# Optimization experiments

Hardware: AMD Instinct MI355X
Metric: run time of the kernel (lower is better)

Reference implementation:

```python
import jax, jax.numpy as jnp
import numpy as np

NEG_CLAMP = -100.0  # torch BCE clamps log terms at -100


def cxcywh_to_xyxy(b):
    cx, cy, w, h = b[..., 0], b[..., 1], b[..., 2], b[..., 3]
    return jnp.stack([cx - 0.5 * w, cy - 0.5 * h, cx + 0.5 * w, cy + 0.5 * h], axis=-1)


def generalized_box_iou(a, b):
    # a: [N,4], b: [T,4] in xyxy
    area_a = (a[:, 2] - a[:, 0]) * (a[:, 3] - a[:, 1])
    area_b = (b[:, 2] - b[:, 0]) * (b[:, 3] - b[:, 1])
    lt = jnp.maximum(a[:, None, :2], b[None, :, :2])
    rb = jnp.minimum(a[:, None, 2:], b[None, :, 2:])
    wh = jnp.clip(rb - lt, 0.0)
    inter = wh[..., 0] * wh[..., 1]
    union = area_a[:, None] + area_b[None, :] - inter
    iou = inter / union
    ltc = jnp.minimum(a[:, None, :2], b[None, :, :2])
    rbc = jnp.maximum(a[:, None, 2:], b[None, :, 2:])
    whc = jnp.clip(rbc - ltc, 0.0)
    areac = whc[..., 0] * whc[..., 1]
    return iou - (areac - union) / areac


def setup_inputs() -> dict:
    key = jax.random.key(0)
    k0, k1, k2, k3, k4, k5 = jax.random.split(key, 6)
    bs, Q, C = 4, 300, 80
    T = 200  # 50 targets per image
    H = W = 160
    H2 = W2 = 320
    pred_logits = jax.random.normal(k0, (bs, Q, C), dtype=jnp.float32)
    pred_boxes = jax.random.uniform(k1, (bs, Q, 4), dtype=jnp.float32, minval=0.02, maxval=0.98)
    pred_masks = jax.random.normal(k2, (bs, Q, H, W), dtype=jnp.float32)
    tgt_ids = jax.random.randint(k3, (T,), 0, C)
    tgt_bbox = jax.random.uniform(k4, (T, 4), dtype=jnp.float32, minval=0.02, maxval=0.98)
    tgt_masks = jnp.round(jax.random.uniform(k5, (T, H2, W2), dtype=jnp.float32))  # binary masks
    return {"pred_logits": pred_logits, "pred_boxes": pred_boxes, "pred_masks": pred_masks,
            "tgt_ids": tgt_ids, "tgt_bbox": tgt_bbox, "tgt_masks": tgt_masks}


def reference(pred_logits, pred_boxes, pred_masks, tgt_ids, tgt_bbox, tgt_masks):
    cost_class_w, cost_bbox_w, cost_giou_w, cost_mask_w, cost_dice_w = 2.0, 5.0, 2.0, 2.0, 2.0
    bs, Q = pred_logits.shape[:2]
    N = bs * Q
    T = tgt_bbox.shape[0]

    out_prob = jax.nn.sigmoid(pred_logits.reshape(N, -1))      # [N, C]
    out_bbox = pred_boxes.reshape(N, 4)

    cost_class = -out_prob[:, tgt_ids]                           # [N, T] gather
    cost_bbox = jnp.abs(out_bbox[:, None, :] - tgt_bbox[None, :, :]).sum(-1)  # L1 cdist
    cost_giou = -generalized_box_iou(cxcywh_to_xyxy(out_bbox), cxcywh_to_xyxy(tgt_bbox))

    C = cost_bbox_w * cost_bbox + cost_giou_w * cost_giou + cost_class_w * cost_class

    # mask costs
    H, W = pred_masks.shape[-2:]
    HW = H * W
    out_logits = pred_masks.reshape(N, HW)
    out_flat = jax.nn.sigmoid(out_logits)                        # [N, HW]
    tgt_resized = jax.image.resize(tgt_masks, (T, H, W), method='bilinear')  # align_corners=False
    tgt_flat = tgt_resized.reshape(T, HW)

    numerator = 2.0 * (out_flat @ tgt_flat.T)                    # [N, T]
    denominator = out_flat.sum(-1)[:, None] + tgt_flat.sum(-1)[None, :]
    cost_dice = -(numerator + 1.0) / (jnp.clip(denominator, 1e-6) + 1.0)

    # BCE mean over pixels as pairwise matmuls (same math as the expanded torch version)
    log_p = jnp.maximum(jax.nn.log_sigmoid(out_logits), NEG_CLAMP)       # log(p)
    log_1mp = jnp.maximum(jax.nn.log_sigmoid(-out_logits), NEG_CLAMP)    # log(1-p)
    cost_mask = -(log_p @ tgt_flat.T + log_1mp @ (1.0 - tgt_flat).T) / HW

    C = C + cost_mask_w * cost_mask + cost_dice_w * cost_dice
    return C.reshape(bs, Q, T)
```

## Files before the change

kernel.cpp:

```cpp
#include <hip/hip_runtime.h>
#include <math.h>

#define N_PRED 1200
#define N_TGT  200
#define T_PAD  208
#define NCLS   80
#define W_OUT  160
#define W_IN   320
#define HW     25600
#define K_TOT  25600
#define KS     25
#define K_CHUNK 1024
#define BK     64
#define MT     19
#define LDA    72
#define LDB    72

typedef __bf16 bf16x8 __attribute__((ext_vector_type(8)));
typedef float  f32x4  __attribute__((ext_vector_type(4)));

__device__ __forceinline__ unsigned short f2bf(float f) {
    unsigned int u = __float_as_uint(f);
    u = u + 0x7FFFu + ((u >> 16) & 1u);
    return (unsigned short)(u >> 16);
}

__device__ __forceinline__ void taps(int i, int& i0, float w[4]) {
    if (i == 0)            { i0 = 0;       w[0]=3.f/7.f; w[1]=3.f/7.f; w[2]=1.f/7.f; w[3]=0.f; }
    else if (i == W_OUT-1) { i0 = 2*i - 2; w[0]=0.f;     w[1]=1.f/7.f; w[2]=3.f/7.f; w[3]=3.f/7.f; }
    else                   { i0 = 2*i - 1; w[0]=0.125f;  w[1]=0.375f;  w[2]=0.375f;  w[3]=0.125f; }
}

__global__ void resize_kernel(const float* __restrict__ tm,
                              unsigned short* __restrict__ tgt_bf,
                              float* __restrict__ tgt_sum) {
    const int t = blockIdx.y, q = blockIdx.x, tid = threadIdx.x;
    if (t >= N_TGT) {
        uint4 z = make_uint4(0,0,0,0);
        uint4* dst = (uint4*)(tgt_bf + (size_t)t * HW) + q * (HW/8/4);
        for (int u = tid; u < HW/8/4; u += 256) dst[u] = z;
        return;
    }
    const float* src = tm + (size_t)t * (W_IN * W_IN);
    float part = 0.f;
    const int p0 = q * (HW/4);
    for (int pp = tid; pp < HW/4; pp += 256) {
        const int p = p0 + pp;
        const int i = p / W_OUT, j = p % W_OUT;
        int r0, c0; float wr[4], wc[4];
        taps(i, r0, wr); taps(j, c0, wc);
        float v = 0.f;
        #pragma unroll
        for (int a = 0; a < 4; a++) {
            const float* row = src + (size_t)(r0 + a) * W_IN + c0;
            float h = wc[0]*row[0] + wc[1]*row[1] + wc[2]*row[2] + wc[3]*row[3];
            v += wr[a] * h;
        }
        tgt_bf[(size_t)t * HW + p] = f2bf(v);
        part += v;
    }
    __shared__ float red[256];
    red[tid] = part; __syncthreads();
    for (int s = 128; s > 0; s >>= 1) { if (tid < s) red[tid] += red[tid + s]; __syncthreads(); }
    if (tid == 0) atomicAdd(&tgt_sum[t], red[0]);
}

__global__ void rowsum_kernel(const float* __restrict__ pm,
                              float* __restrict__ sig_rs,
                              float* __restrict__ l1p_rs) {
    const int n = blockIdx.x, tid = threadIdx.x;
    const float* row = pm + (size_t)n * HW;
    float s = 0.f, l = 0.f;
    #pragma unroll
    for (int i = 0; i < 25; i++) {
        float4 x4 = *(const float4*)(row + tid * 4 + i * 1024);
        float xs[4] = {x4.x, x4.y, x4.z, x4.w};
        #pragma unroll
        for (int e = 0; e < 4; e++) {
            const float xv = xs[e];
            const float t  = __expf(-fabsf(xv));
            const float inv = __builtin_amdgcn_rcpf(1.f + t);
            s += (xv >= 0.f) ? inv : (1.f - inv);
            l -= __logf(1.f + t) + fmaxf(xv, 0.f);
        }
    }
    __shared__ float redS[256], redL[256];
    redS[tid] = s; redL[tid] = l; __syncthreads();
    for (int st = 128; st > 0; st >>= 1) {
        if (tid < st) { redS[tid] += redS[tid + st]; redL[tid] += redL[tid + st]; }
        __syncthreads();
    }
    if (tid == 0) { sig_rs[n] = redS[0]; l1p_rs[n] = redL[0]; }
}

#define DECL13(p) f32x4 p##0={0,0,0,0}, p##1={0,0,0,0}, p##2={0,0,0,0}, p##3={0,0,0,0}, \
    p##4={0,0,0,0}, p##5={0,0,0,0}, p##6={0,0,0,0}, p##7={0,0,0,0}, p##8={0,0,0,0}, \
    p##9={0,0,0,0}, p##10={0,0,0,0}, p##11={0,0,0,0}, p##12={0,0,0,0}

#define STEP(tt) { bf16x8 b = *(const bf16x8*)&ldsB[((tt)*16 + l16) * LDB + koff]; \
    accS##tt = __builtin_amdgcn_mfma_f32_16x16x32_bf16(aS, b, accS##tt, 0, 0, 0); \
    accX##tt = __builtin_amdgcn_mfma_f32_16x16x32_bf16(aX, b, accX##tt, 0, 0, 0); }

#define CONVW(J, RA) { \
    const float x0 = RA.x, x1 = RA.y, x2 = RA.z, x3 = RA.w; \
    const float s0 = __builtin_amdgcn_rcpf(1.f + __expf(-x0)); \
    const float s1 = __builtin_amdgcn_rcpf(1.f + __expf(-x1)); \
    const float s2 = __builtin_amdgcn_rcpf(1.f + __expf(-x2)); \
    const float s3 = __builtin_amdgcn_rcpf(1.f + __expf(-x3)); \
    const unsigned px0 = (unsigned)f2bf(x0) | ((unsigned)f2bf(x1) << 16); \
    const unsigned px1 = (unsigned)f2bf(x2) | ((unsigned)f2bf(x3) << 16); \
    const unsigned ps0 = (unsigned)f2bf(s0) | ((unsigned)f2bf(s1) << 16); \
    const unsigned ps1 = (unsigned)f2bf(s2) | ((unsigned)f2bf(s3) << 16); \
    *(uint2*)&ldsAX[((J)*16 + arow) * LDA + ac * 4] = make_uint2(px0, px1); \
    *(uint2*)&ldsAS[((J)*16 + arow) * LDA + ac * 4] = make_uint2(ps0, ps1); }

#define EPI(tt) { const size_t b0 = base + (size_t)(wave * 16 + quad * 4) * T_PAD + (tt) * 16 + l16; \
    P1[b0] = accS##tt[0]; P1[b0 + T_PAD] = accS##tt[1]; \
    P1[b0 + 2*T_PAD] = accS##tt[2]; P1[b0 + 3*T_PAD] = accS##tt[3]; \
    P2[b0] = accX##tt[0]; P2[b0 + T_PAD] = accX##tt[1]; \
    P2[b0 + 2*T_PAD] = accX##tt[2]; P2[b0 + 3*T_PAD] = accX##tt[3]; }

__global__ __launch_bounds__(256, 2)
void gemm_kernel(const float* __restrict__ pm,
                 const unsigned short* __restrict__ tgt_bf,
                 float* __restrict__ P1, float* __restrict__ P2) {
    const int ks = blockIdx.x, mtile = blockIdx.y;
    const int tid = threadIdx.x;
    const int wave = tid >> 6, lane = tid & 63;
    const int quad = lane >> 4, l16 = lane & 15;

    __shared__ unsigned short ldsAX[64 * LDA];
    __shared__ unsigned short ldsAS[64 * LDA];
    __shared__ unsigned short ldsB[T_PAD * LDB];

    DECL13(accS);
    DECL13(accX);

    const int m0 = mtile * 64;
    const int arow = tid >> 4;
    const int ac   = tid & 15;
    const int k0   = ks * K_CHUNK;

    int r0i = m0 + 0*16 + arow; if (r0i > N_PRED-1) r0i = N_PRED-1;
    int r1i = m0 + 1*16 + arow; if (r1i > N_PRED-1) r1i = N_PRED-1;
    int r2i = m0 + 2*16 + arow; if (r2i > N_PRED-1) r2i = N_PRED-1;
    int r3i = m0 + 3*16 + arow; if (r3i > N_PRED-1) r3i = N_PRED-1;
    const float* ap0 = pm + (size_t)r0i * K_TOT + ac * 4;
    const float* ap1 = pm + (size_t)r1i * K_TOT + ac * 4;
    const float* ap2 = pm + (size_t)r2i * K_TOT + ac * 4;
    const float* ap3 = pm + (size_t)r3i * K_TOT + ac * 4;

    const int bu  = tid;

    float4 rA0 = *(const float4*)(ap0 + k0);
    float4 rA1 = *(const float4*)(ap1 + k0);
    float4 rA2 = *(const float4*)(ap2 + k0);
    float4 rA3 = *(const float4*)(ap3 + k0);
    uint4 rB0, rB1, rB2, rB3, rB4, rB5, rB6;
    {
        const unsigned short* bp = tgt_bf + k0;
        rB0 = *(const uint4*)(bp + (size_t)((bu       ) >> 3) * K_TOT + ((bu       ) & 7) * 8);
        rB1 = *(const uint4*)(bp + (size_t)((bu +  256) >> 3) * K_TOT + ((bu +  256) & 7) * 8);
        rB2 = *(const uint4*)(bp + (size_t)((bu +  512) >> 3) * K_TOT + ((bu +  512) & 7) * 8);
        rB3 = *(const uint4*)(bp + (size_t)((bu +  768) >> 3) * K_TOT + ((bu +  768) & 7) * 8);
        rB4 = *(const uint4*)(bp + (size_t)((bu + 1024) >> 3) * K_TOT + ((bu + 1024) & 7) * 8);
        rB5 = *(const uint4*)(bp + (size_t)((bu + 1280) >> 3) * K_TOT + ((bu + 1280) & 7) * 8);
        if (tid < 128)
            rB6 = *(const uint4*)(bp + (size_t)((bu + 1536) >> 3) * K_TOT + ((bu + 1536) & 7) * 8);
    }

    for (int ki = 0; ki < K_CHUNK / BK; ki++) {
        __syncthreads();
        CONVW(0, rA0); CONVW(1, rA1); CONVW(2, rA2); CONVW(3, rA3);
        *(uint4*)&ldsB[((bu       ) >> 3) * LDB + ((bu       ) & 7) * 8] = rB0;
        *(uint4*)&ldsB[((bu +  256) >> 3) * LDB + ((bu +  256) & 7) * 8] = rB1;
        *(uint4*)&ldsB[((bu +  512) >> 3) * LDB + ((bu +  512) & 7) * 8] = rB2;
        *(uint4*)&ldsB[((bu +  768) >> 3) * LDB + ((bu +  768) & 7) * 8] = rB3;
        *(uint4*)&ldsB[((bu + 1024) >> 3) * LDB + ((bu + 1024) & 7) * 8] = rB4;
        *(uint4*)&ldsB[((bu + 1280) >> 3) * LDB + ((bu + 1280) & 7) * 8] = rB5;
        if (tid < 128)
            *(uint4*)&ldsB[((bu + 1536) >> 3) * LDB + ((bu + 1536) & 7) * 8] = rB6;
        __syncthreads();
        if (ki != K_CHUNK / BK - 1) {
            const int kn = k0 + (ki + 1) * BK;
            rA0 = *(const float4*)(ap0 + kn);
            rA1 = *(const float4*)(ap1 + kn);
            rA2 = *(const float4*)(ap2 + kn);
            rA3 = *(const float4*)(ap3 + kn);
            const unsigned short* bp = tgt_bf + kn;
            rB0 = *(const uint4*)(bp + (size_t)((bu       ) >> 3) * K_TOT + ((bu       ) & 7) * 8);
            rB1 = *(const uint4*)(bp + (size_t)((bu +  256) >> 3) * K_TOT + ((bu +  256) & 7) * 8);
            rB2 = *(const uint4*)(bp + (size_t)((bu +  512) >> 3) * K_TOT + ((bu +  512) & 7) * 8);
            rB3 = *(const uint4*)(bp + (size_t)((bu +  768) >> 3) * K_TOT + ((bu +  768) & 7) * 8);
            rB4 = *(const uint4*)(bp + (size_t)((bu + 1024) >> 3) * K_TOT + ((bu + 1024) & 7) * 8);
            rB5 = *(const uint4*)(bp + (size_t)((bu + 1280) >> 3) * K_TOT + ((bu + 1280) & 7) * 8);
            if (tid < 128)
                rB6 = *(const uint4*)(bp + (size_t)((bu + 1536) >> 3) * K_TOT + ((bu + 1536) & 7) * 8);
        }
        #pragma unroll
        for (int kk = 0; kk < 2; kk++) {
            const int koff = kk * 32 + quad * 8;
            bf16x8 aX = *(const bf16x8*)&ldsAX[(wave * 16 + l16) * LDA + koff];
            bf16x8 aS = *(const bf16x8*)&ldsAS[(wave * 16 + l16) * LDA + koff];
            STEP(0); STEP(1); STEP(2); STEP(3); STEP(4); STEP(5); STEP(6);
            STEP(7); STEP(8); STEP(9); STEP(10); STEP(11); STEP(12);
        }
    }
    const size_t base = ((size_t)(mtile * KS + ks)) * 64 * T_PAD;
    EPI(0); EPI(1); EPI(2); EPI(3); EPI(4); EPI(5); EPI(6);
    EPI(7); EPI(8); EPI(9); EPI(10); EPI(11); EPI(12);
}

__global__ void combine_kernel(const float* __restrict__ pred_logits,
                               const float* __restrict__ pred_boxes,
                               const int*   __restrict__ tgt_ids,
                               const float* __restrict__ tgt_bbox,
                               const float* __restrict__ P1, const float* __restrict__ P2,
                               const float* __restrict__ sig_rs, const float* __restrict__ l1p_rs,
                               const float* __restrict__ tgt_sum,
                               float* __restrict__ out) {
    const int e = blockIdx.x * 256 + threadIdx.x;
    if (e >= N_PRED * N_TGT) return;
    const int n = e / N_TGT, t = e - n * N_TGT;
    const int mtile = n >> 6, mrow = n & 63;

    const size_t pb = ((size_t)mtile * KS * 64 + mrow) * T_PAD + t;
    float s1 = 0.f, s2 = 0.f;
    for (int ks = 0; ks < KS; ks++) {
        s1 += P1[pb + (size_t)ks * 64 * T_PAD];
        s2 += P2[pb + (size_t)ks * 64 * T_PAD];
    }
    const float denom = sig_rs[n] + tgt_sum[t];
    const float cost_dice = -(2.f * s1 + 1.f) / (fmaxf(denom, 1e-6f) + 1.f);
    const float cost_mask = -(s2 + l1p_rs[n]) / (float)HW;
    const int id = tgt_ids[t];
    const float lg = pred_logits[(size_t)n * NCLS + id];
    const float p = 1.f / (1.f + __expf(-lg));
    const float4 ob = *(const float4*)(pred_boxes + (size_t)n * 4);
    const float4 tb = *(const float4*)(tgt_bbox + (size_t)t * 4);
    const float l1 = fabsf(ob.x - tb.x) + fabsf(ob.y - tb.y) + fabsf(ob.z - tb.z) + fabsf(ob.w - tb.w);
    const float ax0 = ob.x - 0.5f*ob.z, ay0 = ob.y - 0.5f*ob.w;
    const float ax1 = ob.x + 0.5f*ob.z, ay1 = ob.y + 0.5f*ob.w;
    const float bx0 = tb.x - 0.5f*tb.z, by0 = tb.y - 0.5f*tb.w;
    const float bx1 = tb.x + 0.5f*tb.z, by1 = tb.y + 0.5f*tb.w;
    const float areaA = (ax1 - ax0) * (ay1 - ay0);
    const float areaB = (bx1 - bx0) * (by1 - by0);
    const float iw = fmaxf(fminf(ax1, bx1) - fmaxf(ax0, bx0), 0.f);
    const float ih = fmaxf(fminf(ay1, by1) - fmaxf(ay0, by0), 0.f);
    const float inter = iw * ih;
    const float uni = areaA + areaB - inter;
    const float iou = inter / uni;
    const float cw = fmaxf(fmaxf(ax1, bx1) - fminf(ax0, bx0), 0.f);
    const float ch = fmaxf(fmaxf(ay1, by1) - fminf(ay0, by0), 0.f);
    const float areaC = cw * ch;
    const float giou = iou - (areaC - uni) / areaC;

    out[e] = 5.f * l1 + 2.f * (-giou) + 2.f * (-p) + 2.f * cost_mask + 2.f * cost_dice;
}

extern "C" void kernel_launch(void* const* d_in, const int* in_sizes, int n_in,
                              void* d_out, int out_size, void* d_ws, size_t ws_size,
                              hipStream_t stream) {
    const float* pred_logits = (const float*)d_in[0];
    const float* pred_boxes  = (const float*)d_in[1];
    const float* pred_masks  = (const float*)d_in[2];
    const int*   tgt_ids     = (const int*)d_in[3];
    const float* tgt_bbox    = (const float*)d_in[4];
    const float* tgt_masks   = (const float*)d_in[5];
    float* out = (float*)d_out;

    char* ws = (char*)d_ws;
    size_t off = 0;
    unsigned short* tgt_bf = (unsigned short*)(ws + off);
    off += (size_t)T_PAD * K_TOT * sizeof(unsigned short);
    off = (off + 255) & ~(size_t)255;
    float* tgt_sum = (float*)(ws + off);
    float* sig_rs  = tgt_sum + T_PAD;
    float* l1p_rs  = sig_rs + N_PRED;
    off += (size_t)(T_PAD + 2 * N_PRED) * sizeof(float);
    off = (off + 255) & ~(size_t)255;
    float* P1 = (float*)(ws + off);
    off += (size_t)MT * KS * 64 * T_PAD * sizeof(float);
    float* P2 = (float*)(ws + off);
    off += (size_t)MT * KS * 64 * T_PAD * sizeof(float);

    hipMemsetAsync(tgt_sum, 0, T_PAD * sizeof(float), stream);
    hipLaunchKernelGGL(resize_kernel, dim3(4, T_PAD), dim3(256), 0, stream,
                       tgt_masks, tgt_bf, tgt_sum);
    hipLaunchKernelGGL(rowsum_kernel, dim3(N_PRED), dim3(256), 0, stream,
                       pred_masks, sig_rs, l1p_rs);
    hipLaunchKernelGGL(gemm_kernel, dim3(KS, MT), dim3(256), 0, stream,
                       pred_masks, tgt_bf, P1, P2);
    hipLaunchKernelGGL(combine_kernel, dim3((N_PRED * N_TGT + 255) / 256), dim3(256), 0, stream,
                       pred_logits, pred_boxes, tgt_ids, tgt_bbox,
                       P1, P2, sig_rs, l1p_rs, tgt_sum, out);
}
```

Baseline: 311.2 us.

## Fuse mask row sums into GEMM, interleave partials, drop memset and rowsum pass

Removes the separate rowsum kernel, which reread all of pred_masks (about 123 MB), by computing sigmoid and log(1-p) row sums inside the GEMM's A-tile conversion and reducing them with shuffles and atomics. Target mask sums are written as per-quarter partials instead of atomics, so the memset launch goes away. The two GEMM partial buffers are interleaved into one float2 array so the combine kernel does vectorized loads. The cost is extra transcendental math in the GEMM load path, plus atomics on rows that rely on prep_kernel zeroing them first.

```diff
diff --git a/kernel.cpp b/kernel.cpp
--- a/kernel.cpp
+++ b/kernel.cpp
@@ -15,6 +15,7 @@
 #define MT     19
 #define LDA    72
 #define LDB    72
+#define PROW   (2 * T_PAD)
 
 typedef __bf16 bf16x8 __attribute__((ext_vector_type(8)));
 typedef float  f32x4  __attribute__((ext_vector_type(4)));
@@ -31,14 +32,21 @@
     else                   { i0 = 2*i - 1; w[0]=0.125f;  w[1]=0.375f;  w[2]=0.375f;  w[3]=0.125f; }
 }
 
-__global__ void resize_kernel(const float* __restrict__ tm,
-                              unsigned short* __restrict__ tgt_bf,
-                              float* __restrict__ tgt_sum) {
+__global__ void prep_kernel(const float* __restrict__ tm,
+                            unsigned short* __restrict__ tgt_bf,
+                            float* __restrict__ tgt_sumP,
+                            float* __restrict__ sig_rs,
+                            float* __restrict__ l1p_rs) {
     const int t = blockIdx.y, q = blockIdx.x, tid = threadIdx.x;
     if (t >= N_TGT) {
         uint4 z = make_uint4(0,0,0,0);
         uint4* dst = (uint4*)(tgt_bf + (size_t)t * HW) + q * (HW/8/4);
         for (int u = tid; u < HW/8/4; u += 256) dst[u] = z;
+        if (q == 0) {
+            const int base = (t - N_TGT) * 150;
+            if (tid < 150) { sig_rs[base + tid] = 0.f; l1p_rs[base + tid] = 0.f; }
+        }
+        if (tid == 0) tgt_sumP[q * T_PAD + t] = 0.f;
         return;
     }
     const float* src = tm + (size_t)t * (W_IN * W_IN);
@@ -62,35 +70,7 @@
     __shared__ float red[256];
     red[tid] = part; __syncthreads();
     for (int s = 128; s > 0; s >>= 1) { if (tid < s) red[tid] += red[tid + s]; __syncthreads(); }
-    if (tid == 0) atomicAdd(&tgt_sum[t], red[0]);
-}
-
-__global__ void rowsum_kernel(const float* __restrict__ pm,
-                              float* __restrict__ sig_rs,
-                              float* __restrict__ l1p_rs) {
-    const int n = blockIdx.x, tid = threadIdx.x;
-    const float* row = pm + (size_t)n * HW;
-    float s = 0.f, l = 0.f;
-    #pragma unroll
-    for (int i = 0; i < 25; i++) {
-        float4 x4 = *(const float4*)(row + tid * 4 + i * 1024);
-        float xs[4] = {x4.x, x4.y, x4.z, x4.w};
-        #pragma unroll
-        for (int e = 0; e < 4; e++) {
-            const float xv = xs[e];
-            const float t  = __expf(-fabsf(xv));
-            const float inv = __builtin_amdgcn_rcpf(1.f + t);
-            s += (xv >= 0.f) ? inv : (1.f - inv);
-            l -= __logf(1.f + t) + fmaxf(xv, 0.f);
-        }
-    }
-    __shared__ float redS[256], redL[256];
-    redS[tid] = s; redL[tid] = l; __syncthreads();
-    for (int st = 128; st > 0; st >>= 1) {
-        if (tid < st) { redS[tid] += redS[tid + st]; redL[tid] += redL[tid + st]; }
-        __syncthreads();
-    }
-    if (tid == 0) { sig_rs[n] = redS[0]; l1p_rs[n] = redL[0]; }
+    if (tid == 0) tgt_sumP[q * T_PAD + t] = red[0];
 }
 
 #define DECL13(p) f32x4 p##0={0,0,0,0}, p##1={0,0,0,0}, p##2={0,0,0,0}, p##3={0,0,0,0}, \
@@ -103,10 +83,17 @@
 
 #define CONVW(J, RA) { \
     const float x0 = RA.x, x1 = RA.y, x2 = RA.z, x3 = RA.w; \
-    const float s0 = __builtin_amdgcn_rcpf(1.f + __expf(-x0)); \
-    const float s1 = __builtin_amdgcn_rcpf(1.f + __expf(-x1)); \
-    const float s2 = __builtin_amdgcn_rcpf(1.f + __expf(-x2)); \
-    const float s3 = __builtin_amdgcn_rcpf(1.f + __expf(-x3)); \
+    const float t0 = __expf(-fabsf(x0)), t1 = __expf(-fabsf(x1)); \
+    const float t2 = __expf(-fabsf(x2)), t3 = __expf(-fabsf(x3)); \
+    const float i0 = __builtin_amdgcn_rcpf(1.f + t0), i1 = __builtin_amdgcn_rcpf(1.f + t1); \
+    const float i2 = __builtin_amdgcn_rcpf(1.f + t2), i3 = __builtin_amdgcn_rcpf(1.f + t3); \
+    const float s0 = (x0 >= 0.f) ? i0 : 1.f - i0; \
+    const float s1 = (x1 >= 0.f) ? i1 : 1.f - i1; \
+    const float s2 = (x2 >= 0.f) ? i2 : 1.f - i2; \
+    const float s3 = (x3 >= 0.f) ? i3 : 1.f - i3; \
+    sS##J += (s0 + s1) + (s2 + s3); \
+    sL##J -= __logf(1.f + t0) + fmaxf(x0, 0.f) + __logf(1.f + t1) + fmaxf(x1, 0.f) \
+           + __logf(1.f + t2) + fmaxf(x2, 0.f) + __logf(1.f + t3) + fmaxf(x3, 0.f); \
     const unsigned px0 = (unsigned)f2bf(x0) | ((unsigned)f2bf(x1) << 16); \
     const unsigned px1 = (unsigned)f2bf(x2) | ((unsigned)f2bf(x3) << 16); \
     const unsigned ps0 = (unsigned)f2bf(s0) | ((unsigned)f2bf(s1) << 16); \
@@ -114,16 +101,17 @@
     *(uint2*)&ldsAX[((J)*16 + arow) * LDA + ac * 4] = make_uint2(px0, px1); \
     *(uint2*)&ldsAS[((J)*16 + arow) * LDA + ac * 4] = make_uint2(ps0, ps1); }
 
-#define EPI(tt) { const size_t b0 = base + (size_t)(wave * 16 + quad * 4) * T_PAD + (tt) * 16 + l16; \
-    P1[b0] = accS##tt[0]; P1[b0 + T_PAD] = accS##tt[1]; \
-    P1[b0 + 2*T_PAD] = accS##tt[2]; P1[b0 + 3*T_PAD] = accS##tt[3]; \
-    P2[b0] = accX##tt[0]; P2[b0 + T_PAD] = accX##tt[1]; \
-    P2[b0 + 2*T_PAD] = accX##tt[2]; P2[b0 + 3*T_PAD] = accX##tt[3]; }
+#define EPI(tt) { const size_t b0 = base + (size_t)(wave * 16 + quad * 4) * PROW + 2 * ((tt) * 16 + l16); \
+    *(float2*)&P[b0           ] = make_float2(accS##tt[0], accX##tt[0]); \
+    *(float2*)&P[b0 +     PROW] = make_float2(accS##tt[1], accX##tt[1]); \
+    *(float2*)&P[b0 + 2 * PROW] = make_float2(accS##tt[2], accX##tt[2]); \
+    *(float2*)&P[b0 + 3 * PROW] = make_float2(accS##tt[3], accX##tt[3]); }
 
 __global__ __launch_bounds__(256, 2)
 void gemm_kernel(const float* __restrict__ pm,
                  const unsigned short* __restrict__ tgt_bf,
-                 float* __restrict__ P1, float* __restrict__ P2) {
+                 float* __restrict__ P,
+                 float* __restrict__ sig_rs, float* __restrict__ l1p_rs) {
     const int ks = blockIdx.x, mtile = blockIdx.y;
     const int tid = threadIdx.x;
     const int wave = tid >> 6, lane = tid & 63;
@@ -135,6 +123,8 @@
 
     DECL13(accS);
     DECL13(accX);
+    float sS0 = 0.f, sS1 = 0.f, sS2 = 0.f, sS3 = 0.f;
+    float sL0 = 0.f, sL1 = 0.f, sL2 = 0.f, sL3 = 0.f;
 
     const int m0 = mtile * 64;
     const int arow = tid >> 4;
@@ -150,7 +140,7 @@
     const float* ap2 = pm + (size_t)r2i * K_TOT + ac * 4;
     const float* ap3 = pm + (size_t)r3i * K_TOT + ac * 4;
 
-    const int bu  = tid;
+    const int bu = tid;
 
     float4 rA0 = *(const float4*)(ap0 + k0);
     float4 rA1 = *(const float4*)(ap1 + k0);
@@ -206,31 +196,48 @@
             STEP(7); STEP(8); STEP(9); STEP(10); STEP(11); STEP(12);
         }
     }
-    const size_t base = ((size_t)(mtile * KS + ks)) * 64 * T_PAD;
+    const size_t base = ((size_t)(mtile * KS + ks)) * 64 * PROW;
     EPI(0); EPI(1); EPI(2); EPI(3); EPI(4); EPI(5); EPI(6);
     EPI(7); EPI(8); EPI(9); EPI(10); EPI(11); EPI(12);
+
+    #pragma unroll
+    for (int m = 1; m < 16; m <<= 1) {
+        sS0 += __shfl_xor(sS0, m); sS1 += __shfl_xor(sS1, m);
+        sS2 += __shfl_xor(sS2, m); sS3 += __shfl_xor(sS3, m);
+        sL0 += __shfl_xor(sL0, m); sL1 += __shfl_xor(sL1, m);
+        sL2 += __shfl_xor(sL2, m); sL3 += __shfl_xor(sL3, m);
+    }
+    if (l16 == 0) {
+        const int rg0 = m0 + 0*16 + arow, rg1 = m0 + 1*16 + arow;
+        const int rg2 = m0 + 2*16 + arow, rg3 = m0 + 3*16 + arow;
+        if (rg0 < N_PRED) { atomicAdd(sig_rs + rg0, sS0); atomicAdd(l1p_rs + rg0, sL0); }
+        if (rg1 < N_PRED) { atomicAdd(sig_rs + rg1, sS1); atomicAdd(l1p_rs + rg1, sL1); }
+        if (rg2 < N_PRED) { atomicAdd(sig_rs + rg2, sS2); atomicAdd(l1p_rs + rg2, sL2); }
+        if (rg3 < N_PRED) { atomicAdd(sig_rs + rg3, sS3); atomicAdd(l1p_rs + rg3, sL3); }
+    }
 }
 
 __global__ void combine_kernel(const float* __restrict__ pred_logits,
                                const float* __restrict__ pred_boxes,
                                const int*   __restrict__ tgt_ids,
                                const float* __restrict__ tgt_bbox,
-                               const float* __restrict__ P1, const float* __restrict__ P2,
+                               const float* __restrict__ P,
                                const float* __restrict__ sig_rs, const float* __restrict__ l1p_rs,
-                               const float* __restrict__ tgt_sum,
+                               const float* __restrict__ tgt_sumP,
                                float* __restrict__ out) {
     const int e = blockIdx.x * 256 + threadIdx.x;
     if (e >= N_PRED * N_TGT) return;
     const int n = e / N_TGT, t = e - n * N_TGT;
     const int mtile = n >> 6, mrow = n & 63;
 
-    const size_t pb = ((size_t)mtile * KS * 64 + mrow) * T_PAD + t;
+    const size_t pb = ((size_t)mtile * KS * 64 + mrow) * PROW + 2 * t;
     float s1 = 0.f, s2 = 0.f;
     for (int ks = 0; ks < KS; ks++) {
-        s1 += P1[pb + (size_t)ks * 64 * T_PAD];
-        s2 += P2[pb + (size_t)ks * 64 * T_PAD];
-    }
-    const float denom = sig_rs[n] + tgt_sum[t];
+        float2 v = *(const float2*)&P[pb + (size_t)ks * 64 * PROW];
+        s1 += v.x; s2 += v.y;
+    }
+    const float tsum = tgt_sumP[t] + tgt_sumP[T_PAD + t] + tgt_sumP[2*T_PAD + t] + tgt_sumP[3*T_PAD + t];
+    const float denom = sig_rs[n] + tsum;
     const float cost_dice = -(2.f * s1 + 1.f) / (fmaxf(denom, 1e-6f) + 1.f);
     const float cost_mask = -(s2 + l1p_rs[n]) / (float)HW;
     const int id = tgt_ids[t];
@@ -274,24 +281,19 @@
     unsigned short* tgt_bf = (unsigned short*)(ws + off);
     off += (size_t)T_PAD * K_TOT * sizeof(unsigned short);
     off = (off + 255) & ~(size_t)255;
-    float* tgt_sum = (float*)(ws + off);
-    float* sig_rs  = tgt_sum + T_PAD;
-    float* l1p_rs  = sig_rs + N_PRED;
-    off += (size_t)(T_PAD + 2 * N_PRED) * sizeof(float);
+    float* tgt_sumP = (float*)(ws + off);
+    float* sig_rs   = tgt_sumP + 4 * T_PAD;
+    float* l1p_rs   = sig_rs + N_PRED;
+    off += (size_t)(4 * T_PAD + 2 * N_PRED) * sizeof(float);
     off = (off + 255) & ~(size_t)255;
-    float* P1 = (float*)(ws + off);
-    off += (size_t)MT * KS * 64 * T_PAD * sizeof(float);
-    float* P2 = (float*)(ws + off);
-    off += (size_t)MT * KS * 64 * T_PAD * sizeof(float);
-
-    hipMemsetAsync(tgt_sum, 0, T_PAD * sizeof(float), stream);
-    hipLaunchKernelGGL(resize_kernel, dim3(4, T_PAD), dim3(256), 0, stream,
-                       tgt_masks, tgt_bf, tgt_sum);
-    hipLaunchKernelGGL(rowsum_kernel, dim3(N_PRED), dim3(256), 0, stream,
-                       pred_masks, sig_rs, l1p_rs);
+    float* P = (float*)(ws + off);
+    off += (size_t)MT * KS * 64 * PROW * sizeof(float);
+
+    hipLaunchKernelGGL(prep_kernel, dim3(4, T_PAD), dim3(256), 0, stream,
+                       tgt_masks, tgt_bf, tgt_sumP, sig_rs, l1p_rs);
     hipLaunchKernelGGL(gemm_kernel, dim3(KS, MT), dim3(256), 0, stream,
-                       pred_masks, tgt_bf, P1, P2);
+                       pred_masks, tgt_bf, P, sig_rs, l1p_rs);
     hipLaunchKernelGGL(combine_kernel, dim3((N_PRED * N_TGT + 255) / 256), dim3(256), 0, stream,
                        pred_logits, pred_boxes, tgt_ids, tgt_bbox,
-                       P1, P2, sig_rs, l1p_rs, tgt_sum, out);
-}
+                       P, sig_rs, l1p_rs, tgt_sumP, out);
+}
```

After: 285.0 us. -8.4%, faster.
